# Kernel optimization log

Hardware: AMD Instinct MI355X
Metric: run time of the kernel (lower is better)

The kernel has to match this reference:

```python
import jax, jax.numpy as jnp
import numpy as np

UNITS = 64
CHANNEL = 64
L1 = 32
L2 = 32
BATCH = 64


def setup_inputs() -> dict:
    key = jax.random.key(0)
    k1, k2, k3, k4, k5 = jax.random.split(key, 5)
    input_dim = CHANNEL + 3 * UNITS
    inputs = jax.random.normal(k1, (BATCH, CHANNEL, L1, L2), dtype=jnp.float32)
    W = jax.random.normal(k2, (input_dim, UNITS * 7), dtype=jnp.float32) * (1.0 / np.sqrt(input_dim))
    U_rec = jax.random.normal(k3, (UNITS * 3, UNITS), dtype=jnp.float32) * (1.0 / np.sqrt(UNITS * 3))
    bias = jnp.zeros((UNITS * 8,), dtype=jnp.float32)
    W_ij = jax.random.normal(k4, (CHANNEL, UNITS), dtype=jnp.float32) * (1.0 / np.sqrt(CHANNEL))
    return {"inputs": inputs, "W": W, "U_rec": U_rec, "bias": bias, "W_ij": W_ij}


def reference(inputs, W, U_rec, bias, W_ij):
    B, C, l1, l2 = inputs.shape
    u = W_ij.shape[1]
    wr, br = W[:, : 3 * u], bias[: 3 * u]
    wz, bz = W[:, 3 * u : 7 * u], bias[3 * u : 7 * u]
    b_ij = bias[7 * u :]

    # [L1*L2, B, C] scan order: row-major over (i, j), direction 'lt'
    x = jnp.transpose(inputs, (2, 3, 0, 1)).reshape(l1 * l2, B, C)
    states0 = jnp.zeros((l1 + 1, l2 + 1, B, u), dtype=inputs.dtype)  # zero boundary

    def step(carry, xs):
        states, _ = carry
        s_ij, t = xs
        i = t // l2
        j = t % l2
        h_diag = states[i, j]        # [B, u]
        h_top = states[i, j + 1]
        h_left = states[i + 1, j]
        # q = [h_top, h_left, h_diag, s_ij] : [B, 3u + C]
        q = jnp.concatenate([h_top, h_left, h_diag, s_ij], axis=1)
        r = jax.nn.sigmoid(q @ wr + br)                     # [B, 3u]
        z = q @ wz + bz                                     # [B, 4u]
        zg = jax.nn.softmax(z.reshape(B, 4, u), axis=1)     # softmax across 4 gates per unit
        zi, zl, zt, zd = zg[:, 0], zg[:, 1], zg[:, 2], zg[:, 3]
        h_hat = jnp.tanh(
            s_ij @ W_ij + b_ij
            + (r * jnp.concatenate([h_left, h_top, h_diag], axis=1)) @ U_rec
        )
        h_ij = zl * h_left + zt * h_top + zd * h_diag + zi * h_hat
        states = states.at[i + 1, j + 1].set(h_ij)
        return (states, h_ij), None

    tsteps = jnp.arange(l1 * l2)
    (_, h_last), _ = jax.lax.scan(
        step, (states0, jnp.zeros((B, u), dtype=inputs.dtype)), (x, tsteps)
    )
    return h_last
```

## Files before the change

### kernel.cpp

```cpp
#include <hip/hip_runtime.h>
#include <cstdint>
#include <cstddef>


#define LDIM   32
#define BATCH  64
#define UNITS  64
#define CHAN   64
#define NBT    4
#define BT     16
#define TPB    512

typedef _Float16 f16;
typedef _Float16 f16x8 __attribute__((ext_vector_type(8)));
typedef float    f32x4 __attribute__((ext_vector_type(4)));

__global__ __launch_bounds__(TPB, 2) void spatial_gru_kernel(
    const float* __restrict__ x,
    const float* __restrict__ W,
    const float* __restrict__ Urec,
    const float* __restrict__ bias,
    const float* __restrict__ Wij,
    float* __restrict__ out,
    uint32_t* __restrict__ hbuf)
{
    const int bid = blockIdx.x;
    const int row = bid >> 2;
    const int bt  = bid & 3;
    const int b0  = bt * BT;
    const int t   = (int)threadIdx.x;
    const int u   = t & 63;
    const int g   = t >> 6;
    const int l15 = t & 15;
    const int lq  = (t & 63) >> 4;

    __shared__ __attribute__((aligned(16))) f16 qf[BT][328];
    __shared__ __attribute__((aligned(16))) f16 rf[BT][200];
    __shared__ float qs32[BT][260];
    __shared__ float Gsz [BT][260];

    f16x8 wreg[4][8];
    float bias1[4] = {0.f, 0.f, 0.f, 0.f};
    if (g < 7) {
        const int nb = g * 64 + l15;
#pragma unroll
        for (int T = 0; T < 4; ++T) {
            bias1[T] = bias[nb + 16 * T];
#pragma unroll
            for (int s = 0; s < 8; ++s) {
                f16x8 v;
#pragma unroll
                for (int jj = 0; jj < 8; ++jj) {
                    int kk = s * 32 + lq * 8 + jj;
                    v[jj] = (f16)W[(size_t)kk * 448 + nb + 16 * T];
                }
                wreg[T][s] = v;
            }
        }
    }
    f16x8 wreg2[8];
    const int n2 = (g & 3) * 16 + l15;
    {
#pragma unroll
        for (int s = 0; s < 8; ++s) {
            f16x8 v;
#pragma unroll
            for (int jj = 0; jj < 8; ++jj) {
                int kk = s * 32 + lq * 8 + jj;
                float wv = (kk < 192) ? Urec[kk * 64 + n2] : Wij[(kk - 192) * 64 + n2];
                v[jj] = (f16)wv;
            }
            wreg2[s] = v;
        }
    }
    const float bias2 = bias[448 + n2];

    for (int idx = t; idx < 128 * BT; idx += TPB) {
        int b = idx & 15, k = 64 + (idx >> 4);
        qs32[b][k] = 0.f;
        qf[b][k] = (f16)0.f;
    }

    const size_t xb0 = (size_t)(b0 + 2 * g) * 65536 + (size_t)u * 1024 + (size_t)row * 32;
    const size_t xb1 = xb0 + 65536;
    float nx0 = x[xb0], nx1 = x[xb1];
    __syncthreads();

    for (int j = 0; j < LDIM; ++j) {
        const int par = j & 1;
        const int sof = 192 + par * 64;
        const int hTb = par ? 192 : 0;

        qf[2 * g][sof + u]     = (f16)nx0;
        qf[2 * g + 1][sof + u] = (f16)nx1;
        float ht0 = 0.f, ht1 = 0.f;
        f16 hf0 = (f16)0.f, hf1 = (f16)0.f;
        if (row > 0) {
            const uint32_t* sp =
                hbuf + ((((size_t)(row - 1) * LDIM + j) * NBT + bt) << 9) + (u << 3) + g;
            uint32_t w = __hip_atomic_load(sp, __ATOMIC_RELAXED, __HIP_MEMORY_SCOPE_AGENT);
            while ((w & 0x00010001u) != 0x00010001u) {
                __builtin_amdgcn_s_sleep(1);
                w = __hip_atomic_load(sp, __ATOMIC_RELAXED, __HIP_MEMORY_SCOPE_AGENT);
            }
            hf0 = __builtin_bit_cast(f16, (uint16_t)(w & 0xFFFFu));
            hf1 = __builtin_bit_cast(f16, (uint16_t)(w >> 16));
            ht0 = (float)hf0;
            ht1 = (float)hf1;
        }
        qs32[2 * g][hTb + u]     = ht0;  qf[2 * g][u]     = hf0;
        qs32[2 * g + 1][hTb + u] = ht1;  qf[2 * g + 1][u] = hf1;
        __syncthreads();

        if (j < LDIM - 1) { nx0 = x[xb0 + j + 1]; nx1 = x[xb1 + j + 1]; }

        if (g < 7) {
            f32x4 acc[4];
#pragma unroll
            for (int T = 0; T < 4; ++T)
                acc[T] = (f32x4){bias1[T], bias1[T], bias1[T], bias1[T]};
#pragma unroll
            for (int s = 0; s < 8; ++s) {
                const int off = (s < 6) ? s * 32 : sof + (s - 6) * 32;
                f16x8 a = *(const f16x8*)&qf[l15][off + lq * 8];
#pragma unroll
                for (int T = 0; T < 4; ++T)
                    acc[T] = __builtin_amdgcn_mfma_f32_16x16x32_f16(a, wreg[T][s], acc[T], 0, 0, 0);
            }
            if (g < 3) {
                const int colbase = (g == 0) ? 64 : (g == 1) ? hTb : 128;
#pragma unroll
                for (int T = 0; T < 4; ++T)
#pragma unroll
                    for (int r = 0; r < 4; ++r) {
                        float rr = 1.f / (1.f + __expf(-acc[T][r]));
                        int b = lq * 4 + r;
                        float hv = qs32[b][colbase + T * 16 + l15];
                        rf[b][g * 64 + T * 16 + l15] = (f16)(rr * hv);
                    }
            } else {
                const int zb = (g - 3) * 64;
#pragma unroll
                for (int T = 0; T < 4; ++T)
#pragma unroll
                    for (int r = 0; r < 4; ++r)
                        Gsz[lq * 4 + r][zb + T * 16 + l15] = acc[T][r];
            }
        }
        __syncthreads();

        if (g >= 4) {
            f32x4 a2 = (f32x4){bias2, bias2, bias2, bias2};
#pragma unroll
            for (int s = 0; s < 6; ++s) {
                f16x8 a = *(const f16x8*)&rf[l15][s * 32 + lq * 8];
                a2 = __builtin_amdgcn_mfma_f32_16x16x32_f16(a, wreg2[s], a2, 0, 0, 0);
            }
#pragma unroll
            for (int s = 6; s < 8; ++s) {
                f16x8 a = *(const f16x8*)&qf[l15][sof + (s - 6) * 32 + lq * 8];
                a2 = __builtin_amdgcn_mfma_f32_16x16x32_f16(a, wreg2[s], a2, 0, 0, 0);
            }
            uint32_t pk[2] = {0u, 0u};
#pragma unroll
            for (int r = 0; r < 4; ++r) {
                const int b = lq * 4 + r;
                float e2 = __expf(2.f * a2[r]);
                float th = 1.f - 2.f / (e2 + 1.f);
                float zi = Gsz[b][n2],       zl = Gsz[b][64 + n2];
                float zt = Gsz[b][128 + n2], zd = Gsz[b][192 + n2];
                float mx = fmaxf(fmaxf(zi, zl), fmaxf(zt, zd));
                float ei = __expf(zi - mx), el = __expf(zl - mx);
                float et = __expf(zt - mx), ed = __expf(zd - mx);
                float inv = 1.f / (ei + el + et + ed);
                float hT = qs32[b][hTb + n2], hL = qs32[b][64 + n2], hD = qs32[b][128 + n2];
                float hv = (el * hL + et * hT + ed * hD + ei * th) * inv;
                qs32[b][128 + n2] = hT;
                qs32[b][64 + n2]  = hv;
                qf[b][128 + n2] = (f16)hT;
                qf[b][64 + n2]  = (f16)hv;
                if (row == LDIM - 1 && j == LDIM - 1)
                    out[(size_t)(b0 + b) * UNITS + n2] = hv;
                uint32_t h16 = (uint32_t)(__builtin_bit_cast(uint16_t, (f16)hv) | 1u);
                pk[r >> 1] |= h16 << ((r & 1) * 16);
            }
            uint64_t pw = ((uint64_t)pk[1] << 32) | pk[0];
            uint64_t* dst = (uint64_t*)(
                hbuf + ((((size_t)row * LDIM + j) * NBT + bt) << 9) + (n2 << 3) + 2 * lq);
            __hip_atomic_store(dst, pw, __ATOMIC_RELAXED, __HIP_MEMORY_SCOPE_AGENT);
        }
    }
}

extern "C" void kernel_launch(void* const* d_in, const int* in_sizes, int n_in,
                              void* d_out, int out_size, void* d_ws, size_t ws_size,
                              hipStream_t stream) {
    const float* x    = (const float*)d_in[0];
    const float* W    = (const float*)d_in[1];
    const float* Urec = (const float*)d_in[2];
    const float* bias = (const float*)d_in[3];
    const float* Wij  = (const float*)d_in[4];
    float* out = (float*)d_out;

    uint32_t* hbuf = (uint32_t*)d_ws;

    spatial_gru_kernel<<<LDIM * NBT, TPB, 0, stream>>>(
        x, W, Urec, bias, Wij, out, hbuf);
}
```

Baseline: 275.0 us.

## Prefetch top-row states and inputs one step ahead in idle waves

The spin-wait on the previous row's hidden states and the x staging move off the critical path. The idle wave 7 polls and loads h_top for step j+1 during the gate MFMAs, and waves 0-3 stage x for the next step during the candidate phase. This removes one __syncthreads-bounded global wait per step. The state layout in hbuf changes to coalesced 32-bit stores. The z-gate scratch is transposed to avoid bank conflicts, and the tanh MFMA chain is split into two accumulators for ILP. In exchange it adds double-buffered qf regions and more register pressure.

```diff
diff --git a/kernel.cpp b/kernel.cpp
--- a/kernel.cpp
+++ b/kernel.cpp
@@ -4,9 +4,6 @@
 
 
 #define LDIM   32
-#define BATCH  64
-#define UNITS  64
-#define CHAN   64
 #define NBT    4
 #define BT     16
 #define TPB    512
@@ -14,6 +11,9 @@
 typedef _Float16 f16;
 typedef _Float16 f16x8 __attribute__((ext_vector_type(8)));
 typedef float    f32x4 __attribute__((ext_vector_type(4)));
+
+#define LD_AGENT(p)   __hip_atomic_load((p), __ATOMIC_RELAXED, __HIP_MEMORY_SCOPE_AGENT)
+#define ST_AGENT(p,v) __hip_atomic_store((p), (v), __ATOMIC_RELAXED, __HIP_MEMORY_SCOPE_AGENT)
 
 __global__ __launch_bounds__(TPB, 2) void spatial_gru_kernel(
     const float* __restrict__ x,
@@ -25,19 +25,14 @@
     uint32_t* __restrict__ hbuf)
 {
     const int bid = blockIdx.x;
-    const int row = bid >> 2;
-    const int bt  = bid & 3;
-    const int b0  = bt * BT;
-    const int t   = (int)threadIdx.x;
-    const int u   = t & 63;
-    const int g   = t >> 6;
-    const int l15 = t & 15;
-    const int lq  = (t & 63) >> 4;
-
-    __shared__ __attribute__((aligned(16))) f16 qf[BT][328];
+    const int row = bid >> 2, bt = bid & 3, b0 = bt * BT;
+    const int t = (int)threadIdx.x, u = t & 63, g = t >> 6;
+    const int l15 = t & 15, lq = (t & 63) >> 4;
+
+    __shared__ __attribute__((aligned(16))) f16 qf[BT][392];
     __shared__ __attribute__((aligned(16))) f16 rf[BT][200];
     __shared__ float qs32[BT][260];
-    __shared__ float Gsz [BT][260];
+    __shared__ float Gt[256][17];
 
     f16x8 wreg[4][8];
     float bias1[4] = {0.f, 0.f, 0.f, 0.f};
@@ -60,59 +55,69 @@
     }
     f16x8 wreg2[8];
     const int n2 = (g & 3) * 16 + l15;
-    {
-#pragma unroll
-        for (int s = 0; s < 8; ++s) {
-            f16x8 v;
-#pragma unroll
-            for (int jj = 0; jj < 8; ++jj) {
-                int kk = s * 32 + lq * 8 + jj;
-                float wv = (kk < 192) ? Urec[kk * 64 + n2] : Wij[(kk - 192) * 64 + n2];
-                v[jj] = (f16)wv;
-            }
-            wreg2[s] = v;
-        }
+#pragma unroll
+    for (int s = 0; s < 8; ++s) {
+        f16x8 v;
+#pragma unroll
+        for (int jj = 0; jj < 8; ++jj) {
+            int kk = s * 32 + lq * 8 + jj;
+            float wv = (kk < 192) ? Urec[kk * 64 + n2] : Wij[(kk - 192) * 64 + n2];
+            v[jj] = (f16)wv;
+        }
+        wreg2[s] = v;
     }
     const float bias2 = bias[448 + n2];
 
-    for (int idx = t; idx < 128 * BT; idx += TPB) {
-        int b = idx & 15, k = 64 + (idx >> 4);
+    for (int idx = t; idx < 256 * BT; idx += TPB) {
+        int b = idx & 15, k = idx >> 4;
         qs32[b][k] = 0.f;
-        qf[b][k] = (f16)0.f;
-    }
-
-    const size_t xb0 = (size_t)(b0 + 2 * g) * 65536 + (size_t)u * 1024 + (size_t)row * 32;
-    const size_t xb1 = xb0 + 65536;
-    float nx0 = x[xb0], nx1 = x[xb1];
+        qf[b][(k < 192) ? k : (128 + k)] = (f16)0.f;
+    }
     __syncthreads();
 
+    const float* xg = x + (size_t)(b0 + g) * 65536 + (size_t)u * 1024 + (size_t)row * 32;
+    float xv[4] = {0.f, 0.f, 0.f, 0.f};
+    uint32_t wsp[8];
+    if (g < 4) {
+#pragma unroll
+        for (int i = 0; i < 4; ++i)
+            qf[g + 4 * i][192 + u] = (f16)xg[(size_t)i * 4 * 65536];
+#pragma unroll
+        for (int i = 0; i < 4; ++i)
+            xv[i] = xg[(size_t)i * 4 * 65536 + 1];
+    } else if (g == 7 && row > 0) {
+        const uint32_t* hp0 = hbuf + (((size_t)((row - 1) * LDIM) * NBT + bt) << 9) + u;
+        uint32_t w0[8];
+#pragma unroll
+        for (int p = 0; p < 8; ++p) w0[p] = LD_AGENT(hp0 + (p << 6));
+#pragma unroll
+        for (int p = 0; p < 8; ++p)
+            while ((w0[p] & 0x00010001u) != 0x00010001u) {
+                __builtin_amdgcn_s_sleep(1);
+                w0[p] = LD_AGENT(hp0 + (p << 6));
+            }
+#pragma unroll
+        for (int p = 0; p < 8; ++p) {
+            f16 h0 = __builtin_bit_cast(f16, (uint16_t)(w0[p] & 0xFFFFu));
+            f16 h1 = __builtin_bit_cast(f16, (uint16_t)(w0[p] >> 16));
+            qf[2 * p][u] = h0;           qf[2 * p + 1][u] = h1;
+            qs32[2 * p][u] = (float)h0;  qs32[2 * p + 1][u] = (float)h1;
+        }
+        const uint32_t* hp1 = hbuf + (((size_t)((row - 1) * LDIM + 1) * NBT + bt) << 9) + u;
+#pragma unroll
+        for (int p = 0; p < 8; ++p) wsp[p] = LD_AGENT(hp1 + (p << 6));
+    }
+
     for (int j = 0; j < LDIM; ++j) {
-        const int par = j & 1;
-        const int sof = 192 + par * 64;
-        const int hTb = par ? 192 : 0;
-
-        qf[2 * g][sof + u]     = (f16)nx0;
-        qf[2 * g + 1][sof + u] = (f16)nx1;
-        float ht0 = 0.f, ht1 = 0.f;
-        f16 hf0 = (f16)0.f, hf1 = (f16)0.f;
-        if (row > 0) {
-            const uint32_t* sp =
-                hbuf + ((((size_t)(row - 1) * LDIM + j) * NBT + bt) << 9) + (u << 3) + g;
-            uint32_t w = __hip_atomic_load(sp, __ATOMIC_RELAXED, __HIP_MEMORY_SCOPE_AGENT);
-            while ((w & 0x00010001u) != 0x00010001u) {
-                __builtin_amdgcn_s_sleep(1);
-                w = __hip_atomic_load(sp, __ATOMIC_RELAXED, __HIP_MEMORY_SCOPE_AGENT);
-            }
-            hf0 = __builtin_bit_cast(f16, (uint16_t)(w & 0xFFFFu));
-            hf1 = __builtin_bit_cast(f16, (uint16_t)(w >> 16));
-            ht0 = (float)hf0;
-            ht1 = (float)hf1;
-        }
-        qs32[2 * g][hTb + u]     = ht0;  qf[2 * g][u]     = hf0;
-        qs32[2 * g + 1][hTb + u] = ht1;  qf[2 * g + 1][u] = hf1;
+        const int par    = j & 1;
+        const int hTq    = par ? 320 : 0;
+        const int sq     = par ? 256 : 192;
+        const int hT32   = par ? 192 : 0;
+        const int hTq_n  = par ? 0 : 320;
+        const int sq_n   = par ? 192 : 256;
+        const int hT32_n = par ? 0 : 192;
+
         __syncthreads();
-
-        if (j < LDIM - 1) { nx0 = x[xb0 + j + 1]; nx1 = x[xb1 + j + 1]; }
 
         if (g < 7) {
             f32x4 acc[4];
@@ -121,22 +126,21 @@
                 acc[T] = (f32x4){bias1[T], bias1[T], bias1[T], bias1[T]};
 #pragma unroll
             for (int s = 0; s < 8; ++s) {
-                const int off = (s < 6) ? s * 32 : sof + (s - 6) * 32;
+                const int off = (s < 2) ? hTq + 32 * s : (s < 6) ? 32 * s : sq + 32 * (s - 6);
                 f16x8 a = *(const f16x8*)&qf[l15][off + lq * 8];
 #pragma unroll
                 for (int T = 0; T < 4; ++T)
                     acc[T] = __builtin_amdgcn_mfma_f32_16x16x32_f16(a, wreg[T][s], acc[T], 0, 0, 0);
             }
             if (g < 3) {
-                const int colbase = (g == 0) ? 64 : (g == 1) ? hTb : 128;
+                const int colbase = (g == 0) ? 64 : (g == 1) ? hT32 : 128;
 #pragma unroll
                 for (int T = 0; T < 4; ++T)
 #pragma unroll
                     for (int r = 0; r < 4; ++r) {
                         float rr = 1.f / (1.f + __expf(-acc[T][r]));
                         int b = lq * 4 + r;
-                        float hv = qs32[b][colbase + T * 16 + l15];
-                        rf[b][g * 64 + T * 16 + l15] = (f16)(rr * hv);
+                        rf[b][g * 64 + T * 16 + l15] = (f16)(rr * qs32[b][colbase + T * 16 + l15]);
                     }
             } else {
                 const int zb = (g - 3) * 64;
@@ -144,50 +148,83 @@
                 for (int T = 0; T < 4; ++T)
 #pragma unroll
                     for (int r = 0; r < 4; ++r)
-                        Gsz[lq * 4 + r][zb + T * 16 + l15] = acc[T][r];
+                        Gt[zb + T * 16 + l15][lq * 4 + r] = acc[T][r];
+            }
+        } else if (row > 0 && j < LDIM - 1) {
+            const uint32_t* hp = hbuf + (((size_t)((row - 1) * LDIM + (j + 1)) * NBT + bt) << 9) + u;
+#pragma unroll
+            for (int p = 0; p < 8; ++p)
+                while ((wsp[p] & 0x00010001u) != 0x00010001u) {
+                    __builtin_amdgcn_s_sleep(1);
+                    wsp[p] = LD_AGENT(hp + (p << 6));
+                }
+#pragma unroll
+            for (int p = 0; p < 8; ++p) {
+                f16 h0 = __builtin_bit_cast(f16, (uint16_t)(wsp[p] & 0xFFFFu));
+                f16 h1 = __builtin_bit_cast(f16, (uint16_t)(wsp[p] >> 16));
+                qf[2 * p][hTq_n + u] = h0;           qf[2 * p + 1][hTq_n + u] = h1;
+                qs32[2 * p][hT32_n + u] = (float)h0; qs32[2 * p + 1][hT32_n + u] = (float)h1;
             }
         }
         __syncthreads();
 
         if (g >= 4) {
-            f32x4 a2 = (f32x4){bias2, bias2, bias2, bias2};
+            if (g == 7 && row > 0 && j < LDIM - 2) {
+                const uint32_t* hp = hbuf + (((size_t)((row - 1) * LDIM + (j + 2)) * NBT + bt) << 9) + u;
+#pragma unroll
+                for (int p = 0; p < 8; ++p) wsp[p] = LD_AGENT(hp + (p << 6));
+            }
+            f32x4 a0 = (f32x4){bias2, bias2, bias2, bias2};
+            f32x4 a1 = (f32x4){0.f, 0.f, 0.f, 0.f};
 #pragma unroll
             for (int s = 0; s < 6; ++s) {
                 f16x8 a = *(const f16x8*)&rf[l15][s * 32 + lq * 8];
-                a2 = __builtin_amdgcn_mfma_f32_16x16x32_f16(a, wreg2[s], a2, 0, 0, 0);
+                if (s & 1) a1 = __builtin_amdgcn_mfma_f32_16x16x32_f16(a, wreg2[s], a1, 0, 0, 0);
+                else       a0 = __builtin_amdgcn_mfma_f32_16x16x32_f16(a, wreg2[s], a0, 0, 0, 0);
             }
 #pragma unroll
             for (int s = 6; s < 8; ++s) {
-                f16x8 a = *(const f16x8*)&qf[l15][sof + (s - 6) * 32 + lq * 8];
-                a2 = __builtin_amdgcn_mfma_f32_16x16x32_f16(a, wreg2[s], a2, 0, 0, 0);
-            }
-            uint32_t pk[2] = {0u, 0u};
+                f16x8 a = *(const f16x8*)&qf[l15][sq + (s - 6) * 32 + lq * 8];
+                if (s & 1) a1 = __builtin_amdgcn_mfma_f32_16x16x32_f16(a, wreg2[s], a1, 0, 0, 0);
+                else       a0 = __builtin_amdgcn_mfma_f32_16x16x32_f16(a, wreg2[s], a0, 0, 0, 0);
+            }
+            uint32_t pk0 = 0u, pk1 = 0u;
 #pragma unroll
             for (int r = 0; r < 4; ++r) {
                 const int b = lq * 4 + r;
-                float e2 = __expf(2.f * a2[r]);
+                float hh = a0[r] + a1[r];
+                float e2 = __expf(2.f * hh);
                 float th = 1.f - 2.f / (e2 + 1.f);
-                float zi = Gsz[b][n2],       zl = Gsz[b][64 + n2];
-                float zt = Gsz[b][128 + n2], zd = Gsz[b][192 + n2];
+                float zi = Gt[n2][b],       zl = Gt[64 + n2][b];
+                float zt = Gt[128 + n2][b], zd = Gt[192 + n2][b];
                 float mx = fmaxf(fmaxf(zi, zl), fmaxf(zt, zd));
                 float ei = __expf(zi - mx), el = __expf(zl - mx);
                 float et = __expf(zt - mx), ed = __expf(zd - mx);
                 float inv = 1.f / (ei + el + et + ed);
-                float hT = qs32[b][hTb + n2], hL = qs32[b][64 + n2], hD = qs32[b][128 + n2];
+                float hT = qs32[b][hT32 + n2], hL = qs32[b][64 + n2], hD = qs32[b][128 + n2];
                 float hv = (el * hL + et * hT + ed * hD + ei * th) * inv;
-                qs32[b][128 + n2] = hT;
-                qs32[b][64 + n2]  = hv;
-                qf[b][128 + n2] = (f16)hT;
-                qf[b][64 + n2]  = (f16)hv;
+                qs32[b][128 + n2] = hT;   qs32[b][64 + n2] = hv;
+                qf[b][128 + n2] = (f16)hT; qf[b][64 + n2] = (f16)hv;
                 if (row == LDIM - 1 && j == LDIM - 1)
-                    out[(size_t)(b0 + b) * UNITS + n2] = hv;
+                    out[(size_t)(b0 + b) * 64 + n2] = hv;
                 uint32_t h16 = (uint32_t)(__builtin_bit_cast(uint16_t, (f16)hv) | 1u);
-                pk[r >> 1] |= h16 << ((r & 1) * 16);
-            }
-            uint64_t pw = ((uint64_t)pk[1] << 32) | pk[0];
-            uint64_t* dst = (uint64_t*)(
-                hbuf + ((((size_t)row * LDIM + j) * NBT + bt) << 9) + (n2 << 3) + 2 * lq);
-            __hip_atomic_store(dst, pw, __ATOMIC_RELAXED, __HIP_MEMORY_SCOPE_AGENT);
+                if (r & 2) pk1 |= h16 << ((r & 1) * 16);
+                else       pk0 |= h16 << ((r & 1) * 16);
+            }
+            uint32_t* dst = hbuf + (((size_t)(row * LDIM + j) * NBT + bt) << 9) + n2;
+            ST_AGENT(dst + ((2 * lq) << 6),     pk0);
+            ST_AGENT(dst + ((2 * lq + 1) << 6), pk1);
+        } else {
+            if (j < LDIM - 1) {
+#pragma unroll
+                for (int i = 0; i < 4; ++i)
+                    qf[g + 4 * i][sq_n + u] = (f16)xv[i];
+                if (j < LDIM - 2) {
+#pragma unroll
+                    for (int i = 0; i < 4; ++i)
+                        xv[i] = xg[(size_t)i * 4 * 65536 + j + 2];
+                }
+            }
         }
     }
 }
```

Result: slower. 342.7 us (+24.6%).
